# Kernel optimization log

Hardware: AMD Instinct MI355X
Metric: run time of the kernel (lower is better)

## Reference

```python
import jax, jax.numpy as jnp
import numpy as np

_A1 = jnp.array([[1.,0.,0.,0.],[0.,1.,0.,0.],[0.,0.,1.,0.],[0.,0.,0.,1.]], dtype=jnp.float32)
_AI = jnp.array([[0.,-1.,0.,0.],[1.,0.,0.,0.],[0.,0.,0.,-1.],[0.,0.,1.,0.]], dtype=jnp.float32)
_AJ = jnp.array([[0.,0.,-1.,0.],[0.,0.,0.,1.],[1.,0.,0.,0.],[0.,-1.,0.,0.]], dtype=jnp.float32)
_AK = jnp.array([[0.,0.,0.,-1.],[0.,0.,-1.,0.],[0.,1.,0.,0.],[1.,0.,0.,0.]], dtype=jnp.float32)

IN_FEATURES = 1024
OUT_FEATURES = 1024
Q_IN = IN_FEATURES // 4
Q_OUT = OUT_FEATURES // 4

def _xavier_uniform(key, shape, gain=0.5):
    fan_out, fan_in = shape
    limit = gain * float(np.sqrt(6.0 / (fan_in + fan_out)))
    return jax.random.uniform(key, shape, jnp.float32, -limit, limit)

def setup_inputs() -> dict:
    key = jax.random.key(0)
    kx, kr, ki, kj, kk = jax.random.split(key, 5)
    x = jax.random.normal(kx, (8, 4096, IN_FEATURES), dtype=jnp.float32)
    R = _xavier_uniform(kr, (Q_OUT, Q_IN))
    I = _xavier_uniform(ki, (Q_OUT, Q_IN))
    J = _xavier_uniform(kj, (Q_OUT, Q_IN))
    K = _xavier_uniform(kk, (Q_OUT, Q_IN))
    bias = jnp.zeros((OUT_FEATURES,), dtype=jnp.float32)
    return {"x": x, "R": R, "I": I, "J": J, "K": K, "bias": bias}

def _build_weight(R, I, J, K):
    # W = kron(A1,R) + kron(AI,I) + kron(AJ,J) + kron(AK,K), shape (4*q_out, 4*q_in)
    # Assemble as 4x4 signed block grid in one einsum-style broadcast.
    # blocks[a,b] = A1[a,b]*R + AI[a,b]*I + AJ[a,b]*J + AK[a,b]*K
    blocks = (_A1[:, :, None, None] * R + _AI[:, :, None, None] * I
              + _AJ[:, :, None, None] * J + _AK[:, :, None, None] * K)  # [4,4,qo,qi]
    qo, qi = R.shape
    return blocks.transpose(0, 2, 1, 3).reshape(4 * qo, 4 * qi)

def reference(x, R, I, J, K, bias):
    W = _build_weight(R, I, J, K)
    return jnp.einsum('bsi,oi->bso', x, W) + bias
```

## Files before the change

kernel.cpp:

```cpp
#include <hip/hip_runtime.h>
#include <hip/hip_bf16.h>

typedef __attribute__((ext_vector_type(4))) float f32x4;
typedef __attribute__((ext_vector_type(4))) uint u32x4;
typedef __attribute__((ext_vector_type(8))) short bf16x8;

#define BM 128
#define BN 128
#define BK 64
#define NTHREADS 256
#define M_TOTAL 32768
#define N_TOTAL 1024
#define K_TOTAL 1024

__device__ __forceinline__ uint pk2(float a, float b) {
  __hip_bfloat162 h = __float22bfloat162_rn(make_float2(a, b));
  uint u;
  __builtin_memcpy(&u, &h, 4);
  return u;
}

__global__ __launch_bounds__(NTHREADS, 2) void qlin_gemm(
    const float* __restrict__ X, const float* __restrict__ Rm,
    const float* __restrict__ Im, const float* __restrict__ Jm,
    const float* __restrict__ Km, const float* __restrict__ bias,
    float* __restrict__ Y)
{
  const int per = ((M_TOTAL / BM) * (N_TOTAL / BN)) >> 3;
  const int bid = (int)blockIdx.x;
  const int swz = (bid & 7) * per + (bid >> 3);
  const int m0 = (swz >> 3) * BM;
  const int n0 = (swz & 7) * BN;

  const int tid = (int)threadIdx.x;
  const int lane = tid & 63;
  const int wave = tid >> 6;
  const int wm = (wave >> 1) << 6;
  const int wn = (wave & 1) << 6;

  __shared__ __align__(16) ushort smA[BM * BK];
  __shared__ __align__(16) ushort smB[BN * BK];
  char* const cA = (char*)smA;
  char* const cB = (char*)smB;

  const int a_idx = n0 >> 8;
  const int o_src = n0 & 255;

  const int r0 = tid >> 3;
  const int k0 = (tid & 7) << 3;
  const int sbase = r0 * (BK * 2) + ((k0 * 2) ^ ((r0 & 7) << 4));

  f32x4 rA[8], rB[8];
  f32x4 acc[4][4];
#pragma unroll
  for (int i = 0; i < 4; ++i)
#pragma unroll
    for (int j = 0; j < 4; ++j) acc[i][j] = (f32x4)(0.0f);

  const int frow_a0 = wm + (lane & 15);
  const int frow_b0 = wn + (lane & 15);
  const int fkb = (lane >> 4) << 4;

  {
    const float* Bsrc = (a_idx == 0) ? Rm : (a_idx == 1) ? Im : (a_idx == 2) ? Jm : Km;
#pragma unroll
    for (int cc = 0; cc < 4; ++cc) {
      const float* pa = X + (size_t)(m0 + r0 + 32 * cc) * K_TOTAL + k0;
      rA[2 * cc] = *(const f32x4*)pa;
      rA[2 * cc + 1] = *(const f32x4*)(pa + 4);
      const float* pb = Bsrc + (o_src + r0 + 32 * cc) * 256 + k0;
      rB[2 * cc] = *(const f32x4*)pb;
      rB[2 * cc + 1] = *(const f32x4*)(pb + 4);
    }
  }

#pragma unroll 1
  for (int kk0 = 0; kk0 < K_TOTAL; kk0 += BK) {
    __syncthreads();

    {
      const int bsel = kk0 >> 8;
      const uint neg = (0x284Eu >> ((a_idx << 2) | bsel)) & 1u;
#pragma unroll
      for (int cc = 0; cc < 4; ++cc) {
        u32x4 va;
        va[0] = pk2(rA[2 * cc][0], rA[2 * cc][1]);
        va[1] = pk2(rA[2 * cc][2], rA[2 * cc][3]);
        va[2] = pk2(rA[2 * cc + 1][0], rA[2 * cc + 1][1]);
        va[3] = pk2(rA[2 * cc + 1][2], rA[2 * cc + 1][3]);
        *(u32x4*)(cA + sbase + 4096 * cc) = va;
      }
      if (neg) {
#pragma unroll
        for (int cc = 0; cc < 4; ++cc) {
          u32x4 vb;
          vb[0] = pk2(-rB[2 * cc][0], -rB[2 * cc][1]);
          vb[1] = pk2(-rB[2 * cc][2], -rB[2 * cc][3]);
          vb[2] = pk2(-rB[2 * cc + 1][0], -rB[2 * cc + 1][1]);
          vb[3] = pk2(-rB[2 * cc + 1][2], -rB[2 * cc + 1][3]);
          *(u32x4*)(cB + sbase + 4096 * cc) = vb;
        }
      } else {
#pragma unroll
        for (int cc = 0; cc < 4; ++cc) {
          u32x4 vb;
          vb[0] = pk2(rB[2 * cc][0], rB[2 * cc][1]);
          vb[1] = pk2(rB[2 * cc][2], rB[2 * cc][3]);
          vb[2] = pk2(rB[2 * cc + 1][0], rB[2 * cc + 1][1]);
          vb[3] = pk2(rB[2 * cc + 1][2], rB[2 * cc + 1][3]);
          *(u32x4*)(cB + sbase + 4096 * cc) = vb;
        }
      }
    }

    __syncthreads();

    if (kk0 + BK < K_TOTAL) {
      const int kn = kk0 + BK;
      const int si = a_idx ^ (kn >> 8);
      const float* Bsrc = (si == 0) ? Rm : (si == 1) ? Im : (si == 2) ? Jm : Km;
      const int kloc = kn & 255;
#pragma unroll
      for (int cc = 0; cc < 4; ++cc) {
        const float* pa = X + (size_t)(m0 + r0 + 32 * cc) * K_TOTAL + kn + k0;
        rA[2 * cc] = *(const f32x4*)pa;
        rA[2 * cc + 1] = *(const f32x4*)(pa + 4);
        const float* pb = Bsrc + (o_src + r0 + 32 * cc) * 256 + kloc + k0;
        rB[2 * cc] = *(const f32x4*)pb;
        rB[2 * cc + 1] = *(const f32x4*)(pb + 4);
      }
    }

#pragma unroll
    for (int ks = 0; ks < 2; ++ks) {
      const int kb = (ks << 6) + fkb;
      bf16x8 af[4], bfr[4];
#pragma unroll
      for (int mi = 0; mi < 4; ++mi) {
        const int row = frow_a0 + (mi << 4);
        af[mi] = *(const bf16x8*)(cA + row * (BK * 2) + (kb ^ ((row & 7) << 4)));
      }
#pragma unroll
      for (int ni = 0; ni < 4; ++ni) {
        const int row = frow_b0 + (ni << 4);
        bfr[ni] = *(const bf16x8*)(cB + row * (BK * 2) + (kb ^ ((row & 7) << 4)));
      }
#pragma unroll
      for (int mi = 0; mi < 4; ++mi)
#pragma unroll
        for (int ni = 0; ni < 4; ++ni)
          acc[mi][ni] = __builtin_amdgcn_mfma_f32_16x16x32_bf16(
              af[mi], bfr[ni], acc[mi][ni], 0, 0, 0);
    }
  }

#pragma unroll
  for (int ni = 0; ni < 4; ++ni) {
    const int col = n0 + wn + (ni << 4) + (lane & 15);
    const float bv = bias[col];
#pragma unroll
    for (int mi = 0; mi < 4; ++mi) {
      const int r0e = m0 + wm + (mi << 4) + ((lane >> 4) << 2);
#pragma unroll
      for (int j = 0; j < 4; ++j)
        Y[(size_t)(r0e + j) * N_TOTAL + col] = acc[mi][ni][j] + bv;
    }
  }
}

extern "C" void kernel_launch(void* const* d_in, const int* in_sizes, int n_in,
                              void* d_out, int out_size, void* d_ws, size_t ws_size,
                              hipStream_t stream) {
  const float* X = (const float*)d_in[0];
  const float* Rm = (const float*)d_in[1];
  const float* Im = (const float*)d_in[2];
  const float* Jm = (const float*)d_in[3];
  const float* Km = (const float*)d_in[4];
  const float* bias = (const float*)d_in[5];
  float* Y = (float*)d_out;
  dim3 grid((M_TOTAL / BM) * (N_TOTAL / BN));
  qlin_gemm<<<grid, dim3(NTHREADS), 0, stream>>>(X, Rm, Im, Jm, Km, bias, Y);
}
```

Before: 125.4 us.

## Double-buffer LDS tiles to drop one barrier per K step

Shared memory grows to two A/B tile buffers. Each iteration writes tile k+1 into the idle buffer, issues global loads for tile k+2, and runs MFMAs on tile k, with a single __syncthreads per step instead of two. The goal is to overlap the LDS writes and global prefetch with compute and to cut barrier stalls. LDS use doubles to 64KB per block, which could limit the 2-blocks-per-CU occupancy, and register pressure may rise.

```diff
diff --git a/kernel.cpp b/kernel.cpp
--- a/kernel.cpp
+++ b/kernel.cpp
@@ -12,6 +12,7 @@
 #define M_TOTAL 32768
 #define N_TOTAL 1024
 #define K_TOTAL 1024
+#define NSTEPS (K_TOTAL / BK)
 
 __device__ __forceinline__ uint pk2(float a, float b) {
   __hip_bfloat162 h = __float22bfloat162_rn(make_float2(a, b));
@@ -19,6 +20,83 @@
   __builtin_memcpy(&u, &h, 4);
   return u;
 }
+
+
+#define LOAD_TILE(kk) do {                                                    \
+    const int si_ = a_idx ^ ((kk) >> 8);                                      \
+    const float* Bsrc_ = (si_ == 0) ? Rm : (si_ == 1) ? Im                    \
+                       : (si_ == 2) ? Jm : Km;                                \
+    const int kloc_ = (kk) & 255;                                             \
+    _Pragma("unroll")                                                         \
+    for (int cc = 0; cc < 4; ++cc) {                                          \
+      const float* pa_ = X + (size_t)(m0 + r0 + 32 * cc) * K_TOTAL + (kk) + k0;\
+      rA[2 * cc]     = *(const f32x4*)pa_;                                    \
+      rA[2 * cc + 1] = *(const f32x4*)(pa_ + 4);                              \
+      const float* pb_ = Bsrc_ + (o_src + r0 + 32 * cc) * 256 + kloc_ + k0;   \
+      rB[2 * cc]     = *(const f32x4*)pb_;                                    \
+      rB[2 * cc + 1] = *(const f32x4*)(pb_ + 4);                              \
+    }                                                                         \
+  } while (0)
+
+#define COMMIT_TILE(kk, dst) do {                                             \
+    const uint neg_ = (0x284Eu >> ((a_idx << 2) | ((kk) >> 8))) & 1u;         \
+    _Pragma("unroll")                                                         \
+    for (int cc = 0; cc < 4; ++cc) {                                          \
+      u32x4 va_;                                                              \
+      va_[0] = pk2(rA[2 * cc][0], rA[2 * cc][1]);                             \
+      va_[1] = pk2(rA[2 * cc][2], rA[2 * cc][3]);                             \
+      va_[2] = pk2(rA[2 * cc + 1][0], rA[2 * cc + 1][1]);                     \
+      va_[3] = pk2(rA[2 * cc + 1][2], rA[2 * cc + 1][3]);                     \
+      *(u32x4*)((dst) + sbase + 4096 * cc) = va_;                             \
+    }                                                                         \
+    if (neg_) {                                                               \
+      _Pragma("unroll")                                                       \
+      for (int cc = 0; cc < 4; ++cc) {                                        \
+        u32x4 vb_;                                                            \
+        vb_[0] = pk2(-rB[2 * cc][0], -rB[2 * cc][1]);                         \
+        vb_[1] = pk2(-rB[2 * cc][2], -rB[2 * cc][3]);                         \
+        vb_[2] = pk2(-rB[2 * cc + 1][0], -rB[2 * cc + 1][1]);                 \
+        vb_[3] = pk2(-rB[2 * cc + 1][2], -rB[2 * cc + 1][3]);                 \
+        *(u32x4*)((dst) + 16384 + sbase + 4096 * cc) = vb_;                   \
+      }                                                                       \
+    } else {                                                                  \
+      _Pragma("unroll")                                                       \
+      for (int cc = 0; cc < 4; ++cc) {                                        \
+        u32x4 vb_;                                                            \
+        vb_[0] = pk2(rB[2 * cc][0], rB[2 * cc][1]);                           \
+        vb_[1] = pk2(rB[2 * cc][2], rB[2 * cc][3]);                           \
+        vb_[2] = pk2(rB[2 * cc + 1][0], rB[2 * cc + 1][1]);                   \
+        vb_[3] = pk2(rB[2 * cc + 1][2], rB[2 * cc + 1][3]);                   \
+        *(u32x4*)((dst) + 16384 + sbase + 4096 * cc) = vb_;                   \
+      }                                                                       \
+    }                                                                         \
+  } while (0)
+
+#define COMPUTE_TILE(src) do {                                                \
+    _Pragma("unroll")                                                         \
+    for (int ks = 0; ks < 2; ++ks) {                                          \
+      const int kb_ = (ks << 6) + fkb;                                        \
+      bf16x8 af_[4], bf_[4];                                                  \
+      _Pragma("unroll")                                                       \
+      for (int mi = 0; mi < 4; ++mi) {                                        \
+        const int row_ = frow_a0 + (mi << 4);                                 \
+        af_[mi] = *(const bf16x8*)((src) + row_ * (BK * 2)                    \
+                                   + (kb_ ^ ((row_ & 7) << 4)));              \
+      }                                                                       \
+      _Pragma("unroll")                                                       \
+      for (int ni = 0; ni < 4; ++ni) {                                        \
+        const int row_ = frow_b0 + (ni << 4);                                 \
+        bf_[ni] = *(const bf16x8*)((src) + 16384 + row_ * (BK * 2)            \
+                                   + (kb_ ^ ((row_ & 7) << 4)));              \
+      }                                                                       \
+      _Pragma("unroll")                                                       \
+      for (int mi = 0; mi < 4; ++mi)                                          \
+        _Pragma("unroll")                                                     \
+        for (int ni = 0; ni < 4; ++ni)                                        \
+          acc[mi][ni] = __builtin_amdgcn_mfma_f32_16x16x32_bf16(              \
+              af_[mi], bf_[ni], acc[mi][ni], 0, 0, 0);                        \
+    }                                                                         \
+  } while (0)
 
 __global__ __launch_bounds__(NTHREADS, 2) void qlin_gemm(
     const float* __restrict__ X, const float* __restrict__ Rm,
@@ -38,10 +116,8 @@
   const int wm = (wave >> 1) << 6;
   const int wn = (wave & 1) << 6;
 
-  __shared__ __align__(16) ushort smA[BM * BK];
-  __shared__ __align__(16) ushort smB[BN * BK];
-  char* const cA = (char*)smA;
-  char* const cB = (char*)smB;
+  __shared__ __align__(16) ushort sm[2 * 2 * BM * BK];
+  char* const cS = (char*)sm;
 
   const int a_idx = n0 >> 8;
   const int o_src = n0 & 255;
@@ -61,97 +137,19 @@
   const int frow_b0 = wn + (lane & 15);
   const int fkb = (lane >> 4) << 4;
 
-  {
-    const float* Bsrc = (a_idx == 0) ? Rm : (a_idx == 1) ? Im : (a_idx == 2) ? Jm : Km;
-#pragma unroll
-    for (int cc = 0; cc < 4; ++cc) {
-      const float* pa = X + (size_t)(m0 + r0 + 32 * cc) * K_TOTAL + k0;
-      rA[2 * cc] = *(const f32x4*)pa;
-      rA[2 * cc + 1] = *(const f32x4*)(pa + 4);
-      const float* pb = Bsrc + (o_src + r0 + 32 * cc) * 256 + k0;
-      rB[2 * cc] = *(const f32x4*)pb;
-      rB[2 * cc + 1] = *(const f32x4*)(pb + 4);
-    }
-  }
+  LOAD_TILE(0);
+  COMMIT_TILE(0, cS);
+  LOAD_TILE(BK);
+  __syncthreads();
 
 #pragma unroll 1
-  for (int kk0 = 0; kk0 < K_TOTAL; kk0 += BK) {
+  for (int k = 0; k < NSTEPS; ++k) {
+    char* const rbuf = cS + ((k & 1) << 15);
+    char* const wbuf = cS + (((k + 1) & 1) << 15);
+    if (k + 1 < NSTEPS) COMMIT_TILE((k + 1) * BK, wbuf);
+    if (k + 2 < NSTEPS) LOAD_TILE((k + 2) * BK);
+    COMPUTE_TILE(rbuf);
     __syncthreads();
-
-    {
-      const int bsel = kk0 >> 8;
-      const uint neg = (0x284Eu >> ((a_idx << 2) | bsel)) & 1u;
-#pragma unroll
-      for (int cc = 0; cc < 4; ++cc) {
-        u32x4 va;
-        va[0] = pk2(rA[2 * cc][0], rA[2 * cc][1]);
-        va[1] = pk2(rA[2 * cc][2], rA[2 * cc][3]);
-        va[2] = pk2(rA[2 * cc + 1][0], rA[2 * cc + 1][1]);
-        va[3] = pk2(rA[2 * cc + 1][2], rA[2 * cc + 1][3]);
-        *(u32x4*)(cA + sbase + 4096 * cc) = va;
-      }
-      if (neg) {
-#pragma unroll
-        for (int cc = 0; cc < 4; ++cc) {
-          u32x4 vb;
-          vb[0] = pk2(-rB[2 * cc][0], -rB[2 * cc][1]);
-          vb[1] = pk2(-rB[2 * cc][2], -rB[2 * cc][3]);
-          vb[2] = pk2(-rB[2 * cc + 1][0], -rB[2 * cc + 1][1]);
-          vb[3] = pk2(-rB[2 * cc + 1][2], -rB[2 * cc + 1][3]);
-          *(u32x4*)(cB + sbase + 4096 * cc) = vb;
-        }
-      } else {
-#pragma unroll
-        for (int cc = 0; cc < 4; ++cc) {
-          u32x4 vb;
-          vb[0] = pk2(rB[2 * cc][0], rB[2 * cc][1]);
-          vb[1] = pk2(rB[2 * cc][2], rB[2 * cc][3]);
-          vb[2] = pk2(rB[2 * cc + 1][0], rB[2 * cc + 1][1]);
-          vb[3] = pk2(rB[2 * cc + 1][2], rB[2 * cc + 1][3]);
-          *(u32x4*)(cB + sbase + 4096 * cc) = vb;
-        }
-      }
-    }
-
-    __syncthreads();
-
-    if (kk0 + BK < K_TOTAL) {
-      const int kn = kk0 + BK;
-      const int si = a_idx ^ (kn >> 8);
-      const float* Bsrc = (si == 0) ? Rm : (si == 1) ? Im : (si == 2) ? Jm : Km;
-      const int kloc = kn & 255;
-#pragma unroll
-      for (int cc = 0; cc < 4; ++cc) {
-        const float* pa = X + (size_t)(m0 + r0 + 32 * cc) * K_TOTAL + kn + k0;
-        rA[2 * cc] = *(const f32x4*)pa;
-        rA[2 * cc + 1] = *(const f32x4*)(pa + 4);
-        const float* pb = Bsrc + (o_src + r0 + 32 * cc) * 256 + kloc + k0;
-        rB[2 * cc] = *(const f32x4*)pb;
-        rB[2 * cc + 1] = *(const f32x4*)(pb + 4);
-      }
-    }
-
-#pragma unroll
-    for (int ks = 0; ks < 2; ++ks) {
-      const int kb = (ks << 6) + fkb;
-      bf16x8 af[4], bfr[4];
-#pragma unroll
-      for (int mi = 0; mi < 4; ++mi) {
-        const int row = frow_a0 + (mi << 4);
-        af[mi] = *(const bf16x8*)(cA + row * (BK * 2) + (kb ^ ((row & 7) << 4)));
-      }
-#pragma unroll
-      for (int ni = 0; ni < 4; ++ni) {
-        const int row = frow_b0 + (ni << 4);
-        bfr[ni] = *(const bf16x8*)(cB + row * (BK * 2) + (kb ^ ((row & 7) << 4)));
-      }
-#pragma unroll
-      for (int mi = 0; mi < 4; ++mi)
-#pragma unroll
-        for (int ni = 0; ni < 4; ++ni)
-          acc[mi][ni] = __builtin_amdgcn_mfma_f32_16x16x32_bf16(
-              af[mi], bfr[ni], acc[mi][ni], 0, 0, 0);
-    }
   }
 
 #pragma unroll
```

Measured after the change: 124.3 us. Within noise of the previous version (-0.9%).
